# Performance work log

Measured on AMD Instinct MI355X. Metric: run time of the kernel, lower is better.

## Reference

```python
import jax, jax.numpy as jnp
import numpy as np

N_NODES = 100_000
N_EDGES = 1_600_000  # random edges; self-loops appended (add_self_edges_networkx)
IN_FEATS = 64
N_HIDDEN = 64
N_CLASSES = 40


def setup_inputs() -> dict:
    key = jax.random.key(0)
    ks = jax.random.split(key, 10)
    features = jax.random.normal(ks[0], (N_NODES, IN_FEATS), jnp.float32)
    self_loops = jnp.arange(N_NODES, dtype=jnp.int32)
    src = jnp.concatenate([jax.random.randint(ks[1], (N_EDGES,), 0, N_NODES, jnp.int32), self_loops])
    dst = jnp.concatenate([jax.random.randint(ks[2], (N_EDGES,), 0, N_NODES, jnp.int32), self_loops])
    labels = jax.random.randint(ks[3], (N_NODES,), 0, N_CLASSES, jnp.int32)
    mask = jnp.ones((N_NODES,), bool)
    s = 0.05
    W0 = jax.random.normal(ks[4], (IN_FEATS, N_HIDDEN), jnp.float32) * s
    b0 = jnp.zeros((N_HIDDEN,), jnp.float32)
    W1 = jax.random.normal(ks[5], (N_HIDDEN, N_HIDDEN), jnp.float32) * s
    b1 = jnp.zeros((N_HIDDEN,), jnp.float32)
    W2 = jax.random.normal(ks[6], (N_HIDDEN, N_CLASSES), jnp.float32) * s
    b2 = jnp.zeros((N_CLASSES,), jnp.float32)
    return {"features": features, "W0": W0, "b0": b0, "W1": W1, "b1": b1,
            "W2": W2, "b2": b2, "src": src, "dst": dst,
            "labels": labels, "mask": mask}


def reference(features, W0, b0, W1, b1, W2, b2, src, dst, labels, mask):
    # gcn_msg: pass src 'h'; gcn_reduce: sum over incoming messages;
    # NodeApplyModule: linear (+ activation on non-final layers).
    def gcn_layer(h, W, b, act):
        agg = jax.ops.segment_sum(h[src], dst, num_segments=N_NODES)  # gather -> sum reduce
        h = agg @ W + b
        return jax.nn.relu(h) if act else h

    h = gcn_layer(features, W0, b0, act=True)
    h = gcn_layer(h, W1, b1, act=True)
    rep = gcn_layer(h, W2, b2, act=False)  # [N, n_classes]

    # loss: fn_reduce=log_softmax over dim=0 (as written in the source), nll sum / count
    logp = jax.nn.log_softmax(rep, axis=0)
    picked = jnp.take_along_axis(logp, labels[:, None].astype(jnp.int32), axis=1)[:, 0]
    maskf = mask.astype(jnp.float32)
    loss = -jnp.sum(picked * maskf) / jnp.sum(maskf)
    return rep, loss
```

## Files before the change

kernel.cpp:

```cpp
#include <hip/hip_runtime.h>
#include <hip/hip_bf16.h>
#include <hip/hip_fp16.h>

#define NCLS 40

typedef __attribute__((ext_vector_type(8))) _Float16 half8;
typedef __attribute__((ext_vector_type(2))) _Float16 half2h;
union H2U { half2h h; unsigned u; };

#define EPB 16384
#define MAXB1 128
#define MAXNB 104

__global__ void bucket_hist(const int* __restrict__ dst, int E, int nb,
                            int* __restrict__ blockHist) {
    __shared__ int cnt[4][MAXNB];
    int t = threadIdx.x;
    for (int i = t; i < 4 * MAXNB; i += 256) cnt[i / MAXNB][i % MAXNB] = 0;
    __syncthreads();
    int bk = t & 3;
    int base = blockIdx.x * EPB;
    int end = min(base + EPB, E);
    for (int i = base + t; i < end; i += 256) atomicAdd(&cnt[bk][dst[i] >> 10], 1);
    __syncthreads();
    for (int i = t; i < nb; i += 256)
        blockHist[blockIdx.x * nb + i] = cnt[0][i] + cnt[1][i] + cnt[2][i] + cnt[3][i];
}

__global__ void bucket_scan(const int* __restrict__ blockHist, int nB1, int nb,
                            int* __restrict__ blockBase, int* __restrict__ bucketOffs,
                            int* __restrict__ offs, int N, int E, int* __restrict__ red32) {
    __shared__ int h[MAXB1 * MAXNB];
    __shared__ int btot[MAXNB];
    __shared__ int boffs[MAXNB + 1];
    int t = threadIdx.x;
    if (t < 128) red32[t] = 0;
    int total = nB1 * nb;
    for (int i = t; i < total; i += 128) h[i] = blockHist[i];
    __syncthreads();
    for (int b = t; b < nb; b += 128) {
        int run = 0;
        for (int i = 0; i < nB1; ++i) { int v = h[i * nb + b]; h[i * nb + b] = run; run += v; }
        btot[b] = run;
    }
    __syncthreads();
    if (t == 0) {
        int run = 0;
        for (int b = 0; b < nb; ++b) { boffs[b] = run; run += btot[b]; }
        boffs[nb] = run;
    }
    __syncthreads();
    for (int b = t; b < nb; b += 128) {
        int bo = boffs[b];
        for (int i = 0; i < nB1; ++i) h[i * nb + b] += bo;
    }
    __syncthreads();
    for (int i = t; i < total; i += 128) blockBase[i] = h[i];
    for (int b = t; b <= nb; b += 128) bucketOffs[b] = boffs[b];
    if (t == 0) offs[N] = E;
}

__global__ void bucket_place(const int* __restrict__ src, const int* __restrict__ dst, int E,
                             int nb, const int* __restrict__ blockBase,
                             unsigned* __restrict__ tmp) {
    __shared__ int cur[MAXNB];
    int t = threadIdx.x;
    for (int i = t; i < nb; i += 256) cur[i] = blockBase[blockIdx.x * nb + i];
    __syncthreads();
    int base = blockIdx.x * EPB;
    int end = min(base + EPB, E);
    for (int i = base + t; i < end; i += 256) {
        int d = dst[i];
        int s = src[i];
        unsigned pack = ((unsigned)(d & 1023) << 17) | (unsigned)s;
        int pos = atomicAdd(&cur[d >> 10], 1);
        tmp[pos] = pack;
    }
}

__global__ __launch_bounds__(512) void bucket_finalize(const unsigned* __restrict__ tmp,
                                                       const int* __restrict__ bucketOffs,
                                                       int N, int* __restrict__ offs,
                                                       int* __restrict__ esrc) {
    __shared__ int cnt[1024];
    __shared__ int wsum[8];
    int b = blockIdx.x;
    int t = threadIdx.x;
    int bstart = bucketOffs[b], bend = bucketOffs[b + 1];
    cnt[t] = 0;
    cnt[t + 512] = 0;
    __syncthreads();
    for (int i = bstart + t; i < bend; i += 512) atomicAdd(&cnt[tmp[i] >> 17], 1);
    __syncthreads();
    int c0 = cnt[2 * t], c1 = cnt[2 * t + 1];
    int s = c0 + c1;
    int lane = t & 63, w = t >> 6;
    int ssc = s;
    for (int off = 1; off < 64; off <<= 1) {
        int v = __shfl_up(ssc, off, 64);
        if (lane >= off) ssc += v;
    }
    if (lane == 63) wsum[w] = ssc;
    __syncthreads();
    int wo = 0;
#pragma unroll
    for (int k = 0; k < 8; ++k)
        if (k < w) wo += wsum[k];
    int excl = (ssc - s) + wo + bstart;
    __syncthreads();
    int node0 = (b << 10) + 2 * t;
    if (node0 < N) offs[node0] = excl;
    if (node0 + 1 < N) offs[node0 + 1] = excl + c0;
    cnt[2 * t] = excl;
    cnt[2 * t + 1] = excl + c0;
    __syncthreads();
    for (int i = bstart + t; i < bend; i += 512) {
        unsigned p = tmp[i];
        int pos = atomicAdd(&cnt[p >> 17], 1);
        esrc[pos] = (int)(p & 0x1FFFFu);
    }
}

__global__ __launch_bounds__(256) void gemm_fdot(const void* __restrict__ X, int xHalf,
                                                 const float* __restrict__ W,
                                                 const float* __restrict__ bias,
                                                 void* __restrict__ out, int outHalf,
                                                 int N, int FO) {
    int lane = threadIdx.x & 63;
    int waveId = (blockIdx.x * blockDim.x + threadIdx.x) >> 6;
    int nWaves = (gridDim.x * blockDim.x) >> 6;
    int cl = lane < FO ? lane : 0;
    int p = lane & 31;

    H2U wh[32];
#pragma unroll
    for (int j = 0; j < 32; ++j)
        wh[j].h = half2h{(_Float16)W[(2 * j) * FO + cl], (_Float16)W[(2 * j + 1) * FO + cl]};
    float gb = 0.f;
    if (bias != nullptr && lane < FO) gb = bias[lane];

    const unsigned* Xh = (const unsigned*)X;
    const float2* Xf = (const float2*)X;
    float* outF = (float*)out;
    _Float16* outH = (_Float16*)out;

    auto loadX = [&](int row) -> H2U {
        H2U r; r.u = 0;
        if (row < N) {
            if (xHalf) r.u = Xh[(size_t)row * 32 + p];
            else {
                float2 f = Xf[(size_t)row * 32 + p];
                r.h = half2h{(_Float16)f.x, (_Float16)f.y};
            }
        }
        return r;
    };

    int row = waveId;
    H2U xp = loadX(row);
    for (; row < N; row += nWaves) {
        H2U nxt = loadX(row + nWaves);
        float y0 = gb, y1 = 0.f;
#pragma unroll
        for (int j2 = 0; j2 < 32; j2 += 2) {
            H2U r0, r1;
            r0.u = __builtin_amdgcn_readlane(xp.u, j2);
            r1.u = __builtin_amdgcn_readlane(xp.u, j2 + 1);
            y0 = __builtin_amdgcn_fdot2(r0.h, wh[j2].h, y0, false);
            y1 = __builtin_amdgcn_fdot2(r1.h, wh[j2 + 1].h, y1, false);
        }
        float y = y0 + y1;
        if (lane < FO) {
            if (outHalf) outH[(size_t)row * FO + lane] = (_Float16)y;
            else         outF[(size_t)row * FO + lane] = y;
        }
        xp = nxt;
    }
}

__global__ void agg64h_kernel(const _Float16* __restrict__ t, const int* __restrict__ offs,
                              const int* __restrict__ esrc, const float* __restrict__ bias,
                              _Float16* __restrict__ out, int N) {
    int gid = blockIdx.x * blockDim.x + threadIdx.x;
    int node = gid >> 6;
    if (node >= N) return;
    int lane = threadIdx.x & 63;
    int sub = lane >> 3;
    int c8 = lane & 7;
    int beg = offs[node], end = offs[node + 1];
    float a[8];
#pragma unroll
    for (int k = 0; k < 8; ++k) a[k] = 0.f;
    int j = beg + sub;
    for (; j + 8 < end; j += 16) {
        int s0 = esrc[j];
        int s1 = esrc[j + 8];
        half8 v0 = *(const half8*)(t + (size_t)s0 * 64 + c8 * 8);
        half8 v1 = *(const half8*)(t + (size_t)s1 * 64 + c8 * 8);
#pragma unroll
        for (int k = 0; k < 8; ++k) a[k] += (float)v0[k] + (float)v1[k];
    }
    if (j < end) {
        int s0 = esrc[j];
        half8 v0 = *(const half8*)(t + (size_t)s0 * 64 + c8 * 8);
#pragma unroll
        for (int k = 0; k < 8; ++k) a[k] += (float)v0[k];
    }
#pragma unroll
    for (int k = 0; k < 8; ++k) {
        a[k] += __shfl_down(a[k], 32, 64);
        a[k] += __shfl_down(a[k], 16, 64);
        a[k] += __shfl_down(a[k], 8, 64);
    }
    if (sub == 0) {
        half8 hv;
#pragma unroll
        for (int k = 0; k < 8; ++k) {
            float v = fmaxf(a[k] + bias[c8 * 8 + k], 0.f);
            hv[k] = (_Float16)v;
        }
        *(half8*)(out + (size_t)node * 64 + c8 * 8) = hv;
    }
}

__global__ void agg40h_kernel(const _Float16* __restrict__ u, const int* __restrict__ offs,
                              const int* __restrict__ esrc, const float* __restrict__ bias,
                              float* __restrict__ rep, int N) {
    int gid = blockIdx.x * blockDim.x + threadIdx.x;
    int node = gid >> 6;
    if (node >= N) return;
    int lane = threadIdx.x & 63;
    int sub = lane >> 3;
    int c8 = lane & 7;
    int beg = offs[node], end = offs[node + 1];
    float a[8];
#pragma unroll
    for (int k = 0; k < 8; ++k) a[k] = 0.f;
    if (c8 < 5) {
        int j = beg + sub;
        for (; j + 8 < end; j += 16) {
            int s0 = esrc[j];
            int s1 = esrc[j + 8];
            half8 v0 = *(const half8*)(u + (size_t)s0 * 40 + c8 * 8);
            half8 v1 = *(const half8*)(u + (size_t)s1 * 40 + c8 * 8);
#pragma unroll
            for (int k = 0; k < 8; ++k) a[k] += (float)v0[k] + (float)v1[k];
        }
        if (j < end) {
            int s0 = esrc[j];
            half8 v0 = *(const half8*)(u + (size_t)s0 * 40 + c8 * 8);
#pragma unroll
            for (int k = 0; k < 8; ++k) a[k] += (float)v0[k];
        }
    }
#pragma unroll
    for (int k = 0; k < 8; ++k) {
        a[k] += __shfl_down(a[k], 32, 64);
        a[k] += __shfl_down(a[k], 16, 64);
        a[k] += __shfl_down(a[k], 8, 64);
    }
    if (sub == 0 && c8 < 5) {
        float* po = rep + (size_t)node * NCLS + c8 * 8;
        float4 r0, r1;
        r0.x = a[0] + bias[c8 * 8 + 0]; r0.y = a[1] + bias[c8 * 8 + 1];
        r0.z = a[2] + bias[c8 * 8 + 2]; r0.w = a[3] + bias[c8 * 8 + 3];
        r1.x = a[4] + bias[c8 * 8 + 4]; r1.y = a[5] + bias[c8 * 8 + 5];
        r1.z = a[6] + bias[c8 * 8 + 6]; r1.w = a[7] + bias[c8 * 8 + 7];
        *(float4*)(po) = r0;
        *(float4*)(po + 4) = r1;
    }
}

__global__ void loss_pass(const float* __restrict__ rep, const int* __restrict__ labels, int N,
                          double* __restrict__ colSum, double* __restrict__ pickedSum,
                          int* __restrict__ cnt) {
    const int G = 8;
    const int ROWS = 512;
    int t = threadIdx.x;
    int c = t % NCLS;
    int g = t / NCLS;
    int base = blockIdx.x * ROWS;
    int lim = min(base + ROWS, N);
    double sumLoc = 0.0, pickLoc = 0.0;
    int cntLoc = 0;
    for (int r = base + g; r < lim; r += G) {
        float v = rep[(size_t)r * NCLS + c];
        sumLoc += exp((double)v);
        if (labels[r] == c) { pickLoc += (double)v; cntLoc++; }
    }
    __shared__ double colP[G][NCLS];
    __shared__ int cntP[G][NCLS];
    __shared__ double waveP[5];
    colP[g][c] = sumLoc;
    cntP[g][c] = cntLoc;
    __syncthreads();
    if (g == 0) {
        double tot = 0.0;
        int ctot = 0;
        for (int gg = 0; gg < G; ++gg) { tot += colP[gg][c]; ctot += cntP[gg][c]; }
        atomicAdd(&colSum[c], tot);
        if (ctot) atomicAdd(&cnt[c], ctot);
    }
    double wv = pickLoc;
    for (int off = 32; off; off >>= 1) wv += __shfl_down(wv, off, 64);
    if ((t & 63) == 0) waveP[t >> 6] = wv;
    __syncthreads();
    if (t == 0) {
        double s = 0.0;
        for (int i = 0; i < 5; ++i) s += waveP[i];
        atomicAdd(pickedSum, s);
    }
}

__global__ void finalize_kernel(const double* __restrict__ colSum, const int* __restrict__ cnt,
                                const double* __restrict__ pickedSum, int N,
                                float* __restrict__ lossOut) {
    int t = threadIdx.x;
    double term = 0.0;
    if (t < NCLS) term = (double)cnt[t] * log(colSum[t]);
    for (int off = 32; off; off >>= 1) term += __shfl_down(term, off, 64);
    if (t == 0) lossOut[0] = (float)((term - pickedSum[0]) / (double)N);
}

extern "C" void kernel_launch(void* const* d_in, const int* in_sizes, int n_in,
                              void* d_out, int out_size, void* d_ws, size_t ws_size,
                              hipStream_t stream) {
    const float* features = (const float*)d_in[0];
    const float* W0 = (const float*)d_in[1];
    const float* b0 = (const float*)d_in[2];
    const float* W1 = (const float*)d_in[3];
    const float* b1 = (const float*)d_in[4];
    const float* W2 = (const float*)d_in[5];
    const float* b2 = (const float*)d_in[6];
    const int* src = (const int*)d_in[7];
    const int* dst = (const int*)d_in[8];
    const int* labels = (const int*)d_in[9];

    const int N = in_sizes[0] / 64;
    const int E = in_sizes[7];
    const int NC = in_sizes[6];

    char* ws = (char*)d_ws;
    size_t off = 0;
    auto alloc = [&](size_t bytes) -> void* {
        void* p = ws + off;
        off = (off + bytes + 255) & ~(size_t)255;
        return p;
    };
    int* offs      = (int*)alloc((size_t)(N + 1) * 4);
    int* esrc      = (int*)alloc((size_t)E * 4);
    _Float16* bufA = (_Float16*)alloc((size_t)N * 64 * 2);
    _Float16* bufB = (_Float16*)alloc((size_t)N * 64 * 2);
    int* blockHist = (int*)alloc((size_t)MAXB1 * MAXNB * 4);
    int* blockBase = (int*)alloc((size_t)MAXB1 * MAXNB * 4);
    int* bucketOffs= (int*)alloc((size_t)(MAXNB + 1) * 4);
    char* red      = (char*)alloc(512);
    double* colSum    = (double*)red;
    double* pickedSum = (double*)(red + 320);
    int* cntRed       = (int*)(red + 328);

    unsigned* tmp = (unsigned*)bufA;

    float* rep = (float*)d_out;
    float* lossOut = rep + (size_t)N * NC;

    const int nb  = (N + 1023) >> 10;
    const int nB1 = (E + EPB - 1) / EPB;

    bucket_hist<<<nB1, 256, 0, stream>>>(dst, E, nb, blockHist);
    bucket_scan<<<1, 128, 0, stream>>>(blockHist, nB1, nb, blockBase, bucketOffs, offs, N, E,
                                       (int*)red);
    bucket_place<<<nB1, 256, 0, stream>>>(src, dst, E, nb, blockBase, tmp);
    bucket_finalize<<<nb, 512, 0, stream>>>(tmp, bucketOffs, N, offs, esrc);

    const int nodeWaveBlocks = (N * 64 + 255) / 256;

    gemm_fdot<<<2048, 256, 0, stream>>>(features, 0, W0, nullptr, bufA, 1, N, 64);
    agg64h_kernel<<<nodeWaveBlocks, 256, 0, stream>>>(bufA, offs, esrc, b0, bufB, N);
    gemm_fdot<<<2048, 256, 0, stream>>>(bufB, 1, W1, nullptr, bufA, 1, N, 64);
    agg64h_kernel<<<nodeWaveBlocks, 256, 0, stream>>>(bufA, offs, esrc, b1, bufB, N);
    gemm_fdot<<<2048, 256, 0, stream>>>(bufB, 1, W2, nullptr, bufA, 1, N, NC);
    agg40h_kernel<<<nodeWaveBlocks, 256, 0, stream>>>(bufA, offs, esrc, b2, rep, N);

    loss_pass<<<(N + 511) / 512, 320, 0, stream>>>(rep, labels, N, colSum, pickedSum, cntRed);
    finalize_kernel<<<1, 64, 0, stream>>>(colSum, cntRed, pickedSum, N, lossOut);
}
```

Baseline: 400.6 us.

## Fuse bucket histogram with first-layer GEMM and use fdot2 for fp16 accumulation

The first-layer feature transform now runs inside the same launch as the destination-bucket histogram, with extra blocks beyond the histogram blocks doing the GEMM. That removes one kernel launch and lets the two independent jobs overlap. To make this possible, the temporary bucket buffer gets its own workspace allocation instead of aliasing bufA, at the cost of extra workspace memory. The aggregation kernels also replace per-element half-to-float conversions with fdot2 against selector vectors, so each 32-bit word adds two half values into the fp32 accumulators in two instructions.

Measured after the change: 379.5 us. -5.3%, faster.

```diff
diff --git a/kernel.cpp b/kernel.cpp
--- a/kernel.cpp
+++ b/kernel.cpp
@@ -12,19 +12,61 @@
 #define MAXB1 128
 #define MAXNB 104
 
-__global__ void bucket_hist(const int* __restrict__ dst, int E, int nb,
-                            int* __restrict__ blockHist) {
+__global__ __launch_bounds__(256) void hist_and_gemm(
+        const int* __restrict__ dst, int E, int nb, int* __restrict__ blockHist, int nB1,
+        const float* __restrict__ X, const float* __restrict__ W,
+        _Float16* __restrict__ out, int N) {
     __shared__ int cnt[4][MAXNB];
     int t = threadIdx.x;
-    for (int i = t; i < 4 * MAXNB; i += 256) cnt[i / MAXNB][i % MAXNB] = 0;
-    __syncthreads();
-    int bk = t & 3;
-    int base = blockIdx.x * EPB;
-    int end = min(base + EPB, E);
-    for (int i = base + t; i < end; i += 256) atomicAdd(&cnt[bk][dst[i] >> 10], 1);
-    __syncthreads();
-    for (int i = t; i < nb; i += 256)
-        blockHist[blockIdx.x * nb + i] = cnt[0][i] + cnt[1][i] + cnt[2][i] + cnt[3][i];
+    if ((int)blockIdx.x < nB1) {
+        for (int i = t; i < 4 * MAXNB; i += 256) cnt[i / MAXNB][i % MAXNB] = 0;
+        __syncthreads();
+        int bk = t & 3;
+        int base = blockIdx.x * EPB;
+        int end = min(base + EPB, E);
+        for (int i = base + t; i < end; i += 256) atomicAdd(&cnt[bk][dst[i] >> 10], 1);
+        __syncthreads();
+        for (int i = t; i < nb; i += 256)
+            blockHist[blockIdx.x * nb + i] = cnt[0][i] + cnt[1][i] + cnt[2][i] + cnt[3][i];
+        return;
+    }
+    int bid = blockIdx.x - nB1;
+    int nBlocks = gridDim.x - nB1;
+    int lane = t & 63;
+    int waveId = (bid * 256 + t) >> 6;
+    int nWaves = (nBlocks * 256) >> 6;
+    int p = lane & 31;
+
+    H2U wh[32];
+#pragma unroll
+    for (int j = 0; j < 32; ++j)
+        wh[j].h = half2h{(_Float16)W[(2 * j) * 64 + lane], (_Float16)W[(2 * j + 1) * 64 + lane]};
+
+    const float2* Xf = (const float2*)X;
+    auto loadX = [&](int row) -> H2U {
+        H2U r; r.u = 0;
+        if (row < N) {
+            float2 f = Xf[(size_t)row * 32 + p];
+            r.h = half2h{(_Float16)f.x, (_Float16)f.y};
+        }
+        return r;
+    };
+    int row = waveId;
+    H2U xp = loadX(row);
+    for (; row < N; row += nWaves) {
+        H2U nxt = loadX(row + nWaves);
+        float y0 = 0.f, y1 = 0.f;
+#pragma unroll
+        for (int j2 = 0; j2 < 32; j2 += 2) {
+            H2U r0, r1;
+            r0.u = __builtin_amdgcn_readlane(xp.u, j2);
+            r1.u = __builtin_amdgcn_readlane(xp.u, j2 + 1);
+            y0 = __builtin_amdgcn_fdot2(r0.h, wh[j2].h, y0, false);
+            y1 = __builtin_amdgcn_fdot2(r1.h, wh[j2 + 1].h, y1, false);
+        }
+        out[(size_t)row * 64 + lane] = (_Float16)(y0 + y1);
+        xp = nxt;
+    }
 }
 
 __global__ void bucket_scan(const int* __restrict__ blockHist, int nB1, int nb,
@@ -178,6 +220,13 @@
     }
 }
 
+#define ACC_PAIR(word, ae, ao)                                        \
+    do {                                                              \
+        H2U _p; _p.u = (word);                                        \
+        (ae) = __builtin_amdgcn_fdot2(_p.h, selE.h, (ae), false);     \
+        (ao) = __builtin_amdgcn_fdot2(_p.h, selO.h, (ao), false);     \
+    } while (0)
+
 __global__ void agg64h_kernel(const _Float16* __restrict__ t, const int* __restrict__ offs,
                               const int* __restrict__ esrc, const float* __restrict__ bias,
                               _Float16* __restrict__ out, int N) {
@@ -188,6 +237,9 @@
     int sub = lane >> 3;
     int c8 = lane & 7;
     int beg = offs[node], end = offs[node + 1];
+    H2U selE, selO;
+    selE.h = half2h{(_Float16)1.f, (_Float16)0.f};
+    selO.h = half2h{(_Float16)0.f, (_Float16)1.f};
     float a[8];
 #pragma unroll
     for (int k = 0; k < 8; ++k) a[k] = 0.f;
@@ -195,16 +247,18 @@
     for (; j + 8 < end; j += 16) {
         int s0 = esrc[j];
         int s1 = esrc[j + 8];
-        half8 v0 = *(const half8*)(t + (size_t)s0 * 64 + c8 * 8);
-        half8 v1 = *(const half8*)(t + (size_t)s1 * 64 + c8 * 8);
-#pragma unroll
-        for (int k = 0; k < 8; ++k) a[k] += (float)v0[k] + (float)v1[k];
+        uint4 v0 = *(const uint4*)(t + (size_t)s0 * 64 + c8 * 8);
+        uint4 v1 = *(const uint4*)(t + (size_t)s1 * 64 + c8 * 8);
+        ACC_PAIR(v0.x, a[0], a[1]); ACC_PAIR(v0.y, a[2], a[3]);
+        ACC_PAIR(v0.z, a[4], a[5]); ACC_PAIR(v0.w, a[6], a[7]);
+        ACC_PAIR(v1.x, a[0], a[1]); ACC_PAIR(v1.y, a[2], a[3]);
+        ACC_PAIR(v1.z, a[4], a[5]); ACC_PAIR(v1.w, a[6], a[7]);
     }
     if (j < end) {
         int s0 = esrc[j];
-        half8 v0 = *(const half8*)(t + (size_t)s0 * 64 + c8 * 8);
-#pragma unroll
-        for (int k = 0; k < 8; ++k) a[k] += (float)v0[k];
+        uint4 v0 = *(const uint4*)(t + (size_t)s0 * 64 + c8 * 8);
+        ACC_PAIR(v0.x, a[0], a[1]); ACC_PAIR(v0.y, a[2], a[3]);
+        ACC_PAIR(v0.z, a[4], a[5]); ACC_PAIR(v0.w, a[6], a[7]);
     }
 #pragma unroll
     for (int k = 0; k < 8; ++k) {
@@ -233,6 +287,9 @@
     int sub = lane >> 3;
     int c8 = lane & 7;
     int beg = offs[node], end = offs[node + 1];
+    H2U selE, selO;
+    selE.h = half2h{(_Float16)1.f, (_Float16)0.f};
+    selO.h = half2h{(_Float16)0.f, (_Float16)1.f};
     float a[8];
 #pragma unroll
     for (int k = 0; k < 8; ++k) a[k] = 0.f;
@@ -241,16 +298,18 @@
         for (; j + 8 < end; j += 16) {
             int s0 = esrc[j];
             int s1 = esrc[j + 8];
-            half8 v0 = *(const half8*)(u + (size_t)s0 * 40 + c8 * 8);
-            half8 v1 = *(const half8*)(u + (size_t)s1 * 40 + c8 * 8);
-#pragma unroll
-            for (int k = 0; k < 8; ++k) a[k] += (float)v0[k] + (float)v1[k];
+            uint4 v0 = *(const uint4*)(u + (size_t)s0 * 40 + c8 * 8);
+            uint4 v1 = *(const uint4*)(u + (size_t)s1 * 40 + c8 * 8);
+            ACC_PAIR(v0.x, a[0], a[1]); ACC_PAIR(v0.y, a[2], a[3]);
+            ACC_PAIR(v0.z, a[4], a[5]); ACC_PAIR(v0.w, a[6], a[7]);
+            ACC_PAIR(v1.x, a[0], a[1]); ACC_PAIR(v1.y, a[2], a[3]);
+            ACC_PAIR(v1.z, a[4], a[5]); ACC_PAIR(v1.w, a[6], a[7]);
         }
         if (j < end) {
             int s0 = esrc[j];
-            half8 v0 = *(const half8*)(u + (size_t)s0 * 40 + c8 * 8);
-#pragma unroll
-            for (int k = 0; k < 8; ++k) a[k] += (float)v0[k];
+            uint4 v0 = *(const uint4*)(u + (size_t)s0 * 40 + c8 * 8);
+            ACC_PAIR(v0.x, a[0], a[1]); ACC_PAIR(v0.y, a[2], a[3]);
+            ACC_PAIR(v0.z, a[4], a[5]); ACC_PAIR(v0.w, a[6], a[7]);
         }
     }
 #pragma unroll
@@ -351,6 +410,7 @@
     int* esrc      = (int*)alloc((size_t)E * 4);
     _Float16* bufA = (_Float16*)alloc((size_t)N * 64 * 2);
     _Float16* bufB = (_Float16*)alloc((size_t)N * 64 * 2);
+    unsigned* tmp  = (unsigned*)alloc((size_t)E * 4);
     int* blockHist = (int*)alloc((size_t)MAXB1 * MAXNB * 4);
     int* blockBase = (int*)alloc((size_t)MAXB1 * MAXNB * 4);
     int* bucketOffs= (int*)alloc((size_t)(MAXNB + 1) * 4);
@@ -359,15 +419,14 @@
     double* pickedSum = (double*)(red + 320);
     int* cntRed       = (int*)(red + 328);
 
-    unsigned* tmp = (unsigned*)bufA;
-
     float* rep = (float*)d_out;
     float* lossOut = rep + (size_t)N * NC;
 
     const int nb  = (N + 1023) >> 10;
     const int nB1 = (E + EPB - 1) / EPB;
 
-    bucket_hist<<<nB1, 256, 0, stream>>>(dst, E, nb, blockHist);
+    hist_and_gemm<<<nB1 + 2048, 256, 0, stream>>>(dst, E, nb, blockHist, nB1,
+                                                  features, W0, bufA, N);
     bucket_scan<<<1, 128, 0, stream>>>(blockHist, nB1, nb, blockBase, bucketOffs, offs, N, E,
                                        (int*)red);
     bucket_place<<<nB1, 256, 0, stream>>>(src, dst, E, nb, blockBase, tmp);
@@ -375,7 +434,6 @@
 
     const int nodeWaveBlocks = (N * 64 + 255) / 256;
 
-    gemm_fdot<<<2048, 256, 0, stream>>>(features, 0, W0, nullptr, bufA, 1, N, 64);
     agg64h_kernel<<<nodeWaveBlocks, 256, 0, stream>>>(bufA, offs, esrc, b0, bufB, N);
     gemm_fdot<<<2048, 256, 0, stream>>>(bufB, 1, W1, nullptr, bufA, 1, N, 64);
     agg64h_kernel<<<nodeWaveBlocks, 256, 0, stream>>>(bufA, offs, esrc, b1, bufB, N);
```
